# Optimization experiments

Hardware: AMD Instinct MI355X
Metric: run time of the kernel (lower is better)

Reference implementation:

```python
import jax, jax.numpy as jnp
import numpy as np

B, IN, H = 8192, 2048, 2048
EFF = IN + H  # self_recurrent concat of [x_t, state]


def setup_inputs() -> dict:
    key = jax.random.key(0)
    ks = jax.random.split(key, 6)
    s_in = 1.0 / np.sqrt(EFF).astype(np.float32)
    s_h = 1.0 / np.sqrt(H).astype(np.float32)
    return {
        "x_t": jax.random.normal(ks[0], (B, IN), jnp.float32),
        "state": jax.random.normal(ks[1], (B, H), jnp.float32),
        "Wc": jax.random.normal(ks[2], (EFF, H), jnp.float32) * s_in,
        "Uc": jax.random.normal(ks[3], (H, H), jnp.float32) * s_h,
        "bc": jnp.zeros((H,), jnp.float32),
        "Wg": jax.random.normal(ks[4], (EFF, H), jnp.float32) * s_in,
        "Ug": jax.random.normal(ks[5], (H, H), jnp.float32) * s_h,
        "bg": jnp.zeros((H,), jnp.float32),
        "log_step": jnp.zeros((H,), jnp.float32),  # dt_scale=1.0 -> no init shift
        "gamma": jnp.ones((H,), jnp.float32),
        "beta": jnp.zeros((H,), jnp.float32),
    }


def _layernorm(x, gamma, beta, eps=1e-5):
    mu = jnp.mean(x, axis=-1, keepdims=True)
    var = jnp.mean((x - mu) ** 2, axis=-1, keepdims=True)
    return (x - mu) * jax.lax.rsqrt(var + eps) * gamma + beta


def reference(x_t, state, Wc, Uc, bc, Wg, Ug, bg, log_step, gamma, beta):
    dt = 1.0  # step(dt=1.0) * dt_scale(1.0)
    xin = jnp.concatenate([x_t, state], axis=-1)        # [B, EFF], self_recurrent
    cand = jnp.tanh(xin @ Wc + state @ Uc + bc)          # candidate state [B, H]
    gate = jax.nn.sigmoid(xin @ Wg + state @ Ug + bg)    # input gate [B, H]
    tau = jnp.exp(log_step)                              # learned time constant
    alpha = jnp.exp(-dt / tau)                           # exp(-dt/tau) decay
    h_new = alpha * state + (1.0 - alpha) * gate * cand  # liquid gated update
    return _layernorm(h_new, gamma, beta)                # post-norm
```

## Files before the change

kernel.cpp:

```cpp
#include <hip/hip_runtime.h>
#include <hip/hip_bf16.h>
#include <cstdint>
#include <cstddef>

#define Bsz 8192
#define Hdim 2048
#define Kdim 4096
#define Nall 4096

#define BM 128
#define BN 64
#define BK 32

typedef __attribute__((ext_vector_type(8))) short short8;
typedef __attribute__((ext_vector_type(4))) short short4v;
typedef __attribute__((ext_vector_type(4))) float floatx4;

__device__ __forceinline__ short f2bf(float f) {
    unsigned u = __float_as_uint(f);
    unsigned r = (u + 0x7fffu + ((u >> 16) & 1u)) >> 16;
    return (short)(r & 0xffffu);
}

__device__ __forceinline__ float fast_tanh(float x) {
    float e = __expf(2.f * x);
    return 1.f - 2.f / (e + 1.f);
}
__device__ __forceinline__ float fast_sigmoid(float x) {
    return 1.f / (1.f + __expf(-x));
}

__device__ __forceinline__ void g2l16(const void* g, void* l) {
    __builtin_amdgcn_global_load_lds(
        (const __attribute__((address_space(1))) unsigned int*)g,
        (__attribute__((address_space(3))) unsigned int*)l,
        16, 0, 0);
}

__global__ __launch_bounds__(256) void build_wt(
    const float* __restrict__ Wc, const float* __restrict__ Uc,
    const float* __restrict__ Wg, const float* __restrict__ Ug,
    short* __restrict__ Wt)
{
    __shared__ float tile[32][33];
    const int nt = blockIdx.x * 32;
    const int kt = blockIdx.y * 32;
    const int tx = threadIdx.x & 31;
    const int ty = threadIdx.x >> 5;

    const bool isGate = (nt >= Hdim);
    const float* W = isGate ? Wg : Wc;
    const float* U = isGate ? Ug : Uc;
    const int ncol = isGate ? (nt - Hdim) : nt;

#pragma unroll
    for (int r = 0; r < 32; r += 8) {
        int k = kt + ty + r;
        float v = W[(size_t)k * Hdim + ncol + tx];
        if (k >= Hdim) v += U[(size_t)(k - Hdim) * Hdim + ncol + tx];
        tile[ty + r][tx] = v;
    }
    __syncthreads();
    const int nrow = threadIdx.x >> 3;
    const int kg   = threadIdx.x & 7;
    short4v o;
#pragma unroll
    for (int i = 0; i < 4; ++i) o[i] = f2bf(tile[kg * 4 + i][nrow]);
    *(short4v*)&Wt[(size_t)(nt + nrow) * Kdim + kt + kg * 4] = o;
}

__global__ __launch_bounds__(256) void build_acat(
    const float* __restrict__ x, const float* __restrict__ st,
    short* __restrict__ A)
{
    int idx = blockIdx.x * 256 + threadIdx.x;
    int row = idx >> 9;
    int c = (idx & 511) * 8;
    const float* src = (c < Hdim) ? (x + (size_t)row * Hdim + c)
                                  : (st + (size_t)row * Hdim + (c - Hdim));
    float4 v0 = ((const float4*)src)[0];
    float4 v1 = ((const float4*)src)[1];
    short8 o;
    o[0] = f2bf(v0.x); o[1] = f2bf(v0.y); o[2] = f2bf(v0.z); o[3] = f2bf(v0.w);
    o[4] = f2bf(v1.x); o[5] = f2bf(v1.y); o[6] = f2bf(v1.z); o[7] = f2bf(v1.w);
    *(short8*)(A + (size_t)row * Kdim + c) = o;
}

__global__ __launch_bounds__(256, 2) void gemm_fused(
    const short* __restrict__ A,
    const short* __restrict__ Bt,
    const float* __restrict__ st,
    const float* __restrict__ bc, const float* __restrict__ bg,
    const float* __restrict__ lstep,
    float* __restrict__ Hout)
{
    __shared__ __attribute__((aligned(16))) short sA [BM * BK];
    __shared__ __attribute__((aligned(16))) short sBc[BN * BK];
    __shared__ __attribute__((aligned(16))) short sBg[BN * BK];

    const int tid  = threadIdx.x;
    const int lane = tid & 63;
    const int wave = tid >> 6;
    const int wm = wave >> 1;
    const int wn = wave & 1;

    const int m0 = blockIdx.y * BM;
    const int n0 = blockIdx.x * BN;
    const int K = Kdim;

    floatx4 accc[4][2], accg[4][2];
#pragma unroll
    for (int i = 0; i < 4; ++i)
#pragma unroll
        for (int j = 0; j < 2; ++j) {
            floatx4 z = {0.f, 0.f, 0.f, 0.f};
            accc[i][j] = z; accg[i][j] = z;
        }

    const int r0 = tid >> 2;
    const int c0 = ((tid & 3) ^ ((r0 >> 1) & 3)) * 8;
    const short* Ag0 = A  + (size_t)(m0 + r0)        * K + c0;
    const short* Ag1 = A  + (size_t)(m0 + 64 + r0)   * K + c0;
    const short* Bc0 = Bt + (size_t)(n0 + r0)        * K + c0;
    const short* Bg0 = Bt + (size_t)(Hdim + n0 + r0) * K + c0;

    short* dA0 = sA  + wave * 512;
    short* dA1 = sA  + 2048 + wave * 512;
    short* dBc = sBc + wave * 512;
    short* dBg = sBg + wave * 512;

    const int fr = lane & 15;
    const int j4 = lane >> 4;
    const int rslot = (j4 ^ ((fr >> 1) & 3)) * 8;
    const short* sAf  = sA  + (wm * 64 + fr) * BK + rslot;
    const short* sBcf = sBc + (wn * 32 + fr) * BK + rslot;
    const short* sBgf = sBg + (wn * 32 + fr) * BK + rslot;

    for (int k0 = 0; k0 < K; k0 += BK) {
        __syncthreads();
        g2l16(Ag0, dA0); g2l16(Ag1, dA1);
        g2l16(Bc0, dBc); g2l16(Bg0, dBg);
        Ag0 += BK; Ag1 += BK; Bc0 += BK; Bg0 += BK;
        __syncthreads();

        short8 a[4], bcf[2], bgf[2];
#pragma unroll
        for (int i = 0; i < 4; ++i) a[i] = *(const short8*)(sAf + i * 16 * BK);
#pragma unroll
        for (int j = 0; j < 2; ++j) {
            bcf[j] = *(const short8*)(sBcf + j * 16 * BK);
            bgf[j] = *(const short8*)(sBgf + j * 16 * BK);
        }
#pragma unroll
        for (int i = 0; i < 4; ++i)
#pragma unroll
            for (int j = 0; j < 2; ++j) {
                accc[i][j] = __builtin_amdgcn_mfma_f32_16x16x32_bf16(
                    a[i], bcf[j], accc[i][j], 0, 0, 0);
                accg[i][j] = __builtin_amdgcn_mfma_f32_16x16x32_bf16(
                    a[i], bgf[j], accg[i][j], 0, 0, 0);
            }
    }

    const int cn = lane & 15;
    const int cr = (lane >> 4) * 4;
    float bcv[2], bgv[2], alv[2];
#pragma unroll
    for (int j = 0; j < 2; ++j) {
        int col = n0 + wn * 32 + j * 16 + cn;
        bcv[j] = bc[col];
        bgv[j] = bg[col];
        alv[j] = __expf(-__expf(-lstep[col]));
    }
#pragma unroll
    for (int i = 0; i < 4; ++i) {
        int rowb = m0 + wm * 64 + i * 16 + cr;
#pragma unroll
        for (int r = 0; r < 4; ++r) {
            int row = rowb + r;
            const float* sp = st + (size_t)row * Hdim;
            float* hp = Hout + (size_t)row * Hdim;
#pragma unroll
            for (int j = 0; j < 2; ++j) {
                int col = n0 + wn * 32 + j * 16 + cn;
                float cand = fast_tanh(accc[i][j][r] + bcv[j]);
                float gate = fast_sigmoid(accg[i][j][r] + bgv[j]);
                float al = alv[j];
                hp[col] = al * sp[col] + (1.f - al) * gate * cand;
            }
        }
    }
}

__global__ __launch_bounds__(256) void ln_k(
    const float* __restrict__ h, const float* __restrict__ gam,
    const float* __restrict__ bet, float* __restrict__ out)
{
    const int b = blockIdx.x;
    const int t = threadIdx.x;
    const int n0 = t * 8;
    const float* hp = h + (size_t)b * Hdim + n0;

    float4 v0 = ((const float4*)hp)[0];
    float4 v1 = ((const float4*)hp)[1];
    float hv[8] = {v0.x, v0.y, v0.z, v0.w, v1.x, v1.y, v1.z, v1.w};
    float sum = 0.f, ss = 0.f;
#pragma unroll
    for (int i = 0; i < 8; ++i) { sum += hv[i]; ss += hv[i] * hv[i]; }

#pragma unroll
    for (int off = 32; off > 0; off >>= 1) {
        sum += __shfl_down(sum, off);
        ss  += __shfl_down(ss, off);
    }
    __shared__ float red[2][4];
    if ((t & 63) == 0) { red[0][t >> 6] = sum; red[1][t >> 6] = ss; }
    __syncthreads();
    sum = red[0][0] + red[0][1] + red[0][2] + red[0][3];
    ss  = red[1][0] + red[1][1] + red[1][2] + red[1][3];

    const float inv = 1.f / (float)Hdim;
    float mu = sum * inv;
    float var = ss * inv - mu * mu;
    float rs = rsqrtf(var + 1e-5f);

    float* op = out + (size_t)b * Hdim + n0;
#pragma unroll
    for (int i = 0; i < 8; ++i) {
        int n = n0 + i;
        op[i] = (hv[i] - mu) * rs * gam[n] + bet[n];
    }
}

extern "C" void kernel_launch(void* const* d_in, const int* in_sizes, int n_in,
                              void* d_out, int out_size, void* d_ws, size_t ws_size,
                              hipStream_t stream)
{
    const float* x_t   = (const float*)d_in[0];
    const float* state = (const float*)d_in[1];
    const float* Wc    = (const float*)d_in[2];
    const float* Uc    = (const float*)d_in[3];
    const float* bc    = (const float*)d_in[4];
    const float* Wg    = (const float*)d_in[5];
    const float* Ug    = (const float*)d_in[6];
    const float* bg    = (const float*)d_in[7];
    const float* lstep = (const float*)d_in[8];
    const float* gam   = (const float*)d_in[9];
    const float* bet   = (const float*)d_in[10];
    float* out = (float*)d_out;

    char* ws = (char*)d_ws;
    short* Wt   = (short*)ws;
    short* Acat = (short*)(ws + (size_t)32 * 1024 * 1024);
    float* h    = (float*)(ws + (size_t)96 * 1024 * 1024);

    build_wt<<<dim3(Nall / 32, Kdim / 32), 256, 0, stream>>>(Wc, Uc, Wg, Ug, Wt);
    build_acat<<<(Bsz * (Kdim / 8)) / 256, 256, 0, stream>>>(x_t, state, Acat);
    gemm_fused<<<dim3(Hdim / BN, Bsz / BM), 256, 0, stream>>>(
        Acat, Wt, state, bc, bg, lstep, h);
    ln_k<<<Bsz, 256, 0, stream>>>(h, gam, bet, out);
}
```

Measured before the change: 592.8 us.

## Rewrite fused GEMM as 256x256 double-buffered pipelined MFMA kernel

Replaces the 128x64 single-buffered GEMM, which synchronised twice per K step, with a 512-thread block computing a 256-row by 128-column (candidate plus gate) tile over 64-wide K slices. It uses two LDS buffers with interleaved global_load_lds staging, explicit vmcnt/lgkmcnt waits, barriers and s_setprio so loads overlap the MFMA work. A block-index swizzle is added for L2 locality. In exchange it uses much more LDS (128 KB) and more accumulator registers, which may limit occupancy, and the hand-written wait counts must match the number of staged loads exactly to stay correct.

```diff
diff --git a/kernel.cpp b/kernel.cpp
--- a/kernel.cpp
+++ b/kernel.cpp
@@ -8,9 +8,11 @@
 #define Kdim 4096
 #define Nall 4096
 
-#define BM 128
-#define BN 64
-#define BK 32
+#define BM 256
+#define BNH 128
+#define BK 64
+#define NTILES (Kdim / BK)
+#define NITER (NTILES / 2)
 
 typedef __attribute__((ext_vector_type(8))) short short8;
 typedef __attribute__((ext_vector_type(4))) short short4v;
@@ -86,7 +88,50 @@
     *(short8*)(A + (size_t)row * Kdim + c) = o;
 }
 
-__global__ __launch_bounds__(256, 2) void gemm_fused(
+__device__ __forceinline__ void rdA4(const short* base, const int i0,
+                                     short8 (&aF)[4][2],
+                                     const int cs0, const int cs1) {
+#pragma unroll
+    for (int i = 0; i < 4; ++i) {
+        aF[i][0] = *(const short8*)(base + (i0 + i) * 16 * BK + cs0);
+        aF[i][1] = *(const short8*)(base + (i0 + i) * 16 * BK + cs1);
+    }
+}
+__device__ __forceinline__ void rdB2(const short* base, const int j0,
+                                     short8 (&bF)[2][2],
+                                     const int cs0, const int cs1) {
+#pragma unroll
+    for (int j = 0; j < 2; ++j) {
+        bF[j][0] = *(const short8*)(base + (j0 + j) * 16 * BK + cs0);
+        bF[j][1] = *(const short8*)(base + (j0 + j) * 16 * BK + cs1);
+    }
+}
+__device__ __forceinline__ void mma16(floatx4 (&acc)[8][4], const int ia,
+                                      const int jb, const short8 (&aF)[4][2],
+                                      const short8 (&bF)[2][2]) {
+#pragma unroll
+    for (int i = 0; i < 4; ++i)
+#pragma unroll
+        for (int j = 0; j < 2; ++j) {
+            acc[ia + i][jb + j] = __builtin_amdgcn_mfma_f32_16x16x32_bf16(
+                aF[i][0], bF[j][0], acc[ia + i][jb + j], 0, 0, 0);
+            acc[ia + i][jb + j] = __builtin_amdgcn_mfma_f32_16x16x32_bf16(
+                aF[i][1], bF[j][1], acc[ia + i][jb + j], 0, 0, 0);
+        }
+}
+
+#define STAGE(srcArr, h, dstBase, dstOff, koff) do {               \
+    g2l16(srcArr[h][0] + (koff), (dstBase) + dstOff[h][0]);        \
+    g2l16(srcArr[h][1] + (koff), (dstBase) + dstOff[h][1]); } while (0)
+
+#define BAR()   __builtin_amdgcn_s_barrier()
+#define LGKM0() asm volatile("s_waitcnt lgkmcnt(0)" ::: "memory")
+#define VM6()   asm volatile("s_waitcnt vmcnt(6)" ::: "memory")
+#define VM0()   asm volatile("s_waitcnt vmcnt(0)" ::: "memory")
+#define PRIO1() __builtin_amdgcn_s_setprio(1)
+#define PRIO0() __builtin_amdgcn_s_setprio(0)
+
+__global__ __launch_bounds__(512, 2) void gemm_fused(
     const short* __restrict__ A,
     const short* __restrict__ Bt,
     const float* __restrict__ st,
@@ -94,76 +139,131 @@
     const float* __restrict__ lstep,
     float* __restrict__ Hout)
 {
-    __shared__ __attribute__((aligned(16))) short sA [BM * BK];
-    __shared__ __attribute__((aligned(16))) short sBc[BN * BK];
-    __shared__ __attribute__((aligned(16))) short sBg[BN * BK];
+    __shared__ __attribute__((aligned(16))) short lds[4][256 * BK];
+    short* const sA0 = &lds[0][0];
+    short* const sA1 = &lds[1][0];
+    short* const sB0 = &lds[2][0];
+    short* const sB1 = &lds[3][0];
 
     const int tid  = threadIdx.x;
     const int lane = tid & 63;
-    const int wave = tid >> 6;
-    const int wm = wave >> 1;
-    const int wn = wave & 1;
-
-    const int m0 = blockIdx.y * BM;
-    const int n0 = blockIdx.x * BN;
-    const int K = Kdim;
-
-    floatx4 accc[4][2], accg[4][2];
-#pragma unroll
-    for (int i = 0; i < 4; ++i)
-#pragma unroll
-        for (int j = 0; j < 2; ++j) {
-            floatx4 z = {0.f, 0.f, 0.f, 0.f};
-            accc[i][j] = z; accg[i][j] = z;
+    const int w    = tid >> 6;
+    const int wm   = w >> 2;
+    const int wn   = w & 3;
+
+    const int bid = blockIdx.x;
+    const int swz = (bid & 7) * 64 + (bid >> 3);
+    const int m0 = (swz >> 4) * BM;
+    const int n0 = (swz & 15) * BNH;
+
+    const int r8 = lane >> 3;
+    const int c8 = ((lane & 7) ^ r8) * 8;
+    const short* aSrc[2][2];
+    const short* bSrc[2][2];
+    int dstA[2][2], dstB[2][2];
+#pragma unroll
+    for (int h = 0; h < 2; ++h)
+#pragma unroll
+        for (int q = 0; q < 2; ++q) {
+            int f = w * 2 + q;
+            int ra = f * 8 + h * 64 + (f & 8) * 8;
+            int rb = (f >> 2) * 64 + (f & 3) * 8 + h * 32;
+            aSrc[h][q] = A + (size_t)(m0 + ra + r8) * Kdim + c8;
+            int lr = rb + r8;
+            int btrow = n0 + ((lr >> 6) << 5) + (lr & 31)
+                        + ((lr & 32) ? Hdim : 0);
+            bSrc[h][q] = Bt + (size_t)btrow * Kdim + c8;
+            dstA[h][q] = ra * BK;
+            dstB[h][q] = rb * BK;
         }
-
-    const int r0 = tid >> 2;
-    const int c0 = ((tid & 3) ^ ((r0 >> 1) & 3)) * 8;
-    const short* Ag0 = A  + (size_t)(m0 + r0)        * K + c0;
-    const short* Ag1 = A  + (size_t)(m0 + 64 + r0)   * K + c0;
-    const short* Bc0 = Bt + (size_t)(n0 + r0)        * K + c0;
-    const short* Bg0 = Bt + (size_t)(Hdim + n0 + r0) * K + c0;
-
-    short* dA0 = sA  + wave * 512;
-    short* dA1 = sA  + 2048 + wave * 512;
-    short* dBc = sBc + wave * 512;
-    short* dBg = sBg + wave * 512;
 
     const int fr = lane & 15;
     const int j4 = lane >> 4;
-    const int rslot = (j4 ^ ((fr >> 1) & 3)) * 8;
-    const short* sAf  = sA  + (wm * 64 + fr) * BK + rslot;
-    const short* sBcf = sBc + (wn * 32 + fr) * BK + rslot;
-    const short* sBgf = sBg + (wn * 32 + fr) * BK + rslot;
-
-    for (int k0 = 0; k0 < K; k0 += BK) {
-        __syncthreads();
-        g2l16(Ag0, dA0); g2l16(Ag1, dA1);
-        g2l16(Bc0, dBc); g2l16(Bg0, dBg);
-        Ag0 += BK; Ag1 += BK; Bc0 += BK; Bg0 += BK;
-        __syncthreads();
-
-        short8 a[4], bcf[2], bgf[2];
-#pragma unroll
-        for (int i = 0; i < 4; ++i) a[i] = *(const short8*)(sAf + i * 16 * BK);
-#pragma unroll
-        for (int j = 0; j < 2; ++j) {
-            bcf[j] = *(const short8*)(sBcf + j * 16 * BK);
-            bgf[j] = *(const short8*)(sBgf + j * 16 * BK);
+    const int cs0 = ((j4 ^ (fr & 7)) * 8);
+    const int cs1 = (((4 + j4) ^ (fr & 7)) * 8);
+    const short* A0f = sA0 + (wm * 128 + fr) * BK;
+    const short* A1f = sA1 + (wm * 128 + fr) * BK;
+    const short* B0f = sB0 + (wn * 64 + fr) * BK;
+    const short* B1f = sB1 + (wn * 64 + fr) * BK;
+
+    floatx4 acc[8][4];
+#pragma unroll
+    for (int i = 0; i < 8; ++i)
+#pragma unroll
+        for (int j = 0; j < 4; ++j) {
+            floatx4 z = {0.f, 0.f, 0.f, 0.f};
+            acc[i][j] = z;
         }
-#pragma unroll
-        for (int i = 0; i < 4; ++i)
-#pragma unroll
-            for (int j = 0; j < 2; ++j) {
-                accc[i][j] = __builtin_amdgcn_mfma_f32_16x16x32_bf16(
-                    a[i], bcf[j], accc[i][j], 0, 0, 0);
-                accg[i][j] = __builtin_amdgcn_mfma_f32_16x16x32_bf16(
-                    a[i], bgf[j], accg[i][j], 0, 0, 0);
-            }
+    short8 aF[4][2], bLo[2][2], bHi[2][2];
+
+    STAGE(aSrc, 0, sA0, dstA, 0);
+    STAGE(aSrc, 1, sA0, dstA, 0);
+    STAGE(bSrc, 0, sB0, dstB, 0);
+    STAGE(bSrc, 1, sB0, dstB, 0);
+    STAGE(aSrc, 0, sA1, dstA, BK);
+    STAGE(bSrc, 0, sB1, dstB, BK);
+    STAGE(bSrc, 1, sB1, dstB, BK);
+    VM6();
+    BAR();
+
+    for (int it = 0; it < NITER; ++it) {
+        const bool nl = (it < NITER - 1);
+        const int k1  = (2 * it + 1) * BK;
+        const int k02 = (2 * it + 2) * BK;
+        const int k12 = (2 * it + 3) * BK;
+
+        rdA4(A0f, 0, aF, cs0, cs1);
+        rdB2(B0f, 0, bLo, cs0, cs1);
+        STAGE(aSrc, 1, sA1, dstA, k1);
+        BAR(); LGKM0(); PRIO1();
+        mma16(acc, 0, 0, aF, bLo);
+        PRIO0(); BAR();
+
+        rdB2(B0f, 2, bHi, cs0, cs1);
+        if (nl) { STAGE(aSrc, 0, sA0, dstA, k02); }
+        BAR(); LGKM0(); PRIO1();
+        mma16(acc, 0, 2, aF, bHi);
+        PRIO0(); BAR();
+
+        rdA4(A0f, 4, aF, cs0, cs1);
+        if (nl) { STAGE(bSrc, 0, sB0, dstB, k02); }
+        BAR(); LGKM0(); PRIO1();
+        mma16(acc, 4, 0, aF, bLo);
+        PRIO0(); BAR();
+
+        if (nl) { STAGE(bSrc, 1, sB0, dstB, k02); VM6(); }
+        else    { VM0(); }
+        BAR(); PRIO1();
+        mma16(acc, 4, 2, aF, bHi);
+        PRIO0(); BAR();
+
+        rdA4(A1f, 0, aF, cs0, cs1);
+        rdB2(B1f, 0, bLo, cs0, cs1);
+        if (nl) { STAGE(aSrc, 1, sA0, dstA, k02); }
+        BAR(); LGKM0(); PRIO1();
+        mma16(acc, 0, 0, aF, bLo);
+        PRIO0(); BAR();
+
+        rdB2(B1f, 2, bHi, cs0, cs1);
+        if (nl) { STAGE(aSrc, 0, sA1, dstA, k12); }
+        BAR(); LGKM0(); PRIO1();
+        mma16(acc, 0, 2, aF, bHi);
+        PRIO0(); BAR();
+
+        rdA4(A1f, 4, aF, cs0, cs1);
+        if (nl) { STAGE(bSrc, 0, sB1, dstB, k12); }
+        BAR(); LGKM0(); PRIO1();
+        mma16(acc, 4, 0, aF, bLo);
+        PRIO0(); BAR();
+
+        if (nl) { STAGE(bSrc, 1, sB1, dstB, k12); VM6(); }
+        BAR(); PRIO1();
+        mma16(acc, 4, 2, aF, bHi);
+        PRIO0(); BAR();
     }
 
     const int cn = lane & 15;
-    const int cr = (lane >> 4) * 4;
+    const int cr = j4 * 4;
     float bcv[2], bgv[2], alv[2];
 #pragma unroll
     for (int j = 0; j < 2; ++j) {
@@ -173,8 +273,8 @@
         alv[j] = __expf(-__expf(-lstep[col]));
     }
 #pragma unroll
-    for (int i = 0; i < 4; ++i) {
-        int rowb = m0 + wm * 64 + i * 16 + cr;
+    for (int i = 0; i < 8; ++i) {
+        int rowb = m0 + wm * 128 + i * 16 + cr;
 #pragma unroll
         for (int r = 0; r < 4; ++r) {
             int row = rowb + r;
@@ -183,8 +283,8 @@
 #pragma unroll
             for (int j = 0; j < 2; ++j) {
                 int col = n0 + wn * 32 + j * 16 + cn;
-                float cand = fast_tanh(accc[i][j][r] + bcv[j]);
-                float gate = fast_sigmoid(accg[i][j][r] + bgv[j]);
+                float cand = fast_tanh(acc[i][j][r] + bcv[j]);
+                float gate = fast_sigmoid(acc[i][j + 2][r] + bgv[j]);
                 float al = alv[j];
                 hp[col] = al * sp[col] + (1.f - al) * gate * cand;
             }
@@ -256,7 +356,7 @@
 
     build_wt<<<dim3(Nall / 32, Kdim / 32), 256, 0, stream>>>(Wc, Uc, Wg, Ug, Wt);
     build_acat<<<(Bsz * (Kdim / 8)) / 256, 256, 0, stream>>>(x_t, state, Acat);
-    gemm_fused<<<dim3(Hdim / BN, Bsz / BM), 256, 0, stream>>>(
+    gemm_fused<<<dim3((Bsz / BM) * (Hdim / BNH)), 512, 0, stream>>>(
         Acat, Wt, state, bc, bg, lstep, h);
     ln_k<<<Bsz, 256, 0, stream>>>(h, gam, bet, out);
 }
```

Result: faster. 492.8 us (-16.9%).
